# Performance work log

Hardware: AMD Instinct MI355X
Metric: run time of the kernel (lower is better)

The kernel has to match this reference:

```python
import jax, jax.numpy as jnp
import numpy as np

DIM = 1024
NUM_HEADS = 16
HEAD_DIM = DIM // NUM_HEADS
SCALE = HEAD_DIM ** (-0.5)


def alibi_slopes(num_heads):
    x = (2 ** 8) ** (1.0 / num_heads)
    return jnp.array([1.0 / x ** (i + 1) for i in range(num_heads)], dtype=jnp.float32)


def setup_inputs() -> dict:
    key = jax.random.key(0)
    ks = jax.random.split(key, 6)
    B, N = 2, 2048
    x = jax.random.normal(ks[0], (B, N, DIM), dtype=jnp.float32)
    s = DIM ** -0.5
    Wq = jax.random.normal(ks[1], (DIM, DIM), dtype=jnp.float32) * s
    Wk = jax.random.normal(ks[2], (DIM, DIM), dtype=jnp.float32) * s
    Wv = jax.random.normal(ks[3], (DIM, DIM), dtype=jnp.float32) * s
    Wp = jax.random.normal(ks[4], (DIM, DIM), dtype=jnp.float32) * s
    bp = jnp.zeros((DIM,), dtype=jnp.float32)
    return {"x": x, "Wq": Wq, "Wk": Wk, "Wv": Wv, "Wp": Wp, "bp": bp}


def reference(x, Wq, Wk, Wv, Wp, bp):
    B, N, C = x.shape
    H, D = NUM_HEADS, HEAD_DIM
    # Linear layers use torch convention: y = x @ W.T
    q = (x @ Wq.T).reshape(B, N, H, D).transpose(0, 2, 1, 3)  # [B,H,N,D]
    k = (x @ Wk.T).reshape(B, N, H, D).transpose(0, 2, 1, 3)
    v = (x @ Wv.T).reshape(B, N, H, D).transpose(0, 2, 1, 3)
    # ALiBi bias: slopes[h] * (j - i), shape [H,N,N]
    rel = (jnp.arange(N)[None, :] - jnp.arange(N)[:, None]).astype(jnp.float32)
    bias = alibi_slopes(H)[:, None, None] * rel  # [H,N,N]
    # NOTE: original code DIVIDES by scale (= head_dim**-0.5), i.e. multiplies by sqrt(D)
    score = jnp.einsum("bhnd,bhmd->bhnm", q, k) / SCALE + bias[None]
    attn = jax.nn.softmax(score, axis=-1)
    out = jnp.einsum("bhnm,bhmd->bhnd", attn, v)
    out = out.transpose(0, 2, 1, 3).reshape(B, N, C)
    return out @ Wp.T + bp
```

## Files before the change

kernel.cpp:

```cpp
#include <hip/hip_runtime.h>
#include <hip/hip_bf16.h>
#include <cstdint>
#include <cstddef>

#define BB 2
#define NN 2048
#define CC 1024
#define HH 16
#define DD 64
#define MM (BB*NN)

typedef __attribute__((ext_vector_type(8))) _Float16 half8;
typedef __attribute__((ext_vector_type(4))) _Float16 half4;
typedef __attribute__((ext_vector_type(4))) float f32x4;

__device__ __forceinline__ float exp2_fast(float x) {
    float r; asm("v_exp_f32 %0, %1" : "=v"(r) : "v"(x)); return r;
}

__device__ __forceinline__ void gl_lds16(const void* g, void* l) {
    __builtin_amdgcn_global_load_lds(
        (const __attribute__((address_space(1))) unsigned int*)g,
        (__attribute__((address_space(3))) unsigned int*)l, 16, 0, 0);
}

__global__ __launch_bounds__(256) void cvtAll(
    const float* __restrict__ x, const float* __restrict__ wq,
    const float* __restrict__ wk, const float* __restrict__ wv,
    const float* __restrict__ wp, _Float16* __restrict__ X16,
    _Float16* __restrict__ W16) {
    const int NX4 = MM * CC / 4;
    const int NW4 = CC * CC / 4;
    int i = blockIdx.x * 256 + threadIdx.x;
    const float4* src;
    half4* dst;
    if (i < NX4) {
        src = (const float4*)x + i;
        dst = (half4*)X16 + i;
    } else {
        int j = i - NX4;
        int s = j >> 18, off = j & (NW4 - 1);
        const float* wsel = (s == 0) ? wq : (s == 1) ? wk : (s == 2) ? wv : wp;
        src = (const float4*)wsel + off;
        dst = (half4*)(W16 + (size_t)s * CC * CC) + off;
    }
    float4 v = *src;
    half4 h = { (_Float16)v.x, (_Float16)v.y, (_Float16)v.z, (_Float16)v.w };
    *dst = h;
}

__global__ __launch_bounds__(256) void gemmQKV(
    const _Float16* __restrict__ A, const _Float16* __restrict__ B,
    _Float16* __restrict__ QH, _Float16* __restrict__ KH,
    _Float16* __restrict__ VT, float qscale) {
    __shared__ _Float16 sA[128 * 64];
    __shared__ _Float16 sB[128 * 64];
    const int K = CC;

    const int t = threadIdx.x;
    const int id = blockIdx.y * gridDim.x + blockIdx.x;
    const int xcd = id & 7, kk = id >> 3;
    const int bm = xcd * 4 + (kk & 3);
    const int bn = kk >> 2;
    const int w = t >> 6, lane = t & 63;
    const int wr = (w >> 1) * 64, wc = (w & 1) * 64;
    const int lr = lane & 15, lg = lane >> 4;

    f32x4 acc[4][4];
#pragma unroll
    for (int a = 0; a < 4; ++a)
#pragma unroll
        for (int b2 = 0; b2 < 4; ++b2)
#pragma unroll
            for (int e = 0; e < 4; ++e) acc[a][b2][e] = 0.f;

    for (int kt = 0; kt < K; kt += 64) {
#pragma unroll
        for (int p = 0; p < 4; ++p) {
            int u = p * 256 + t;
            int rowu = u >> 3, su = (u & 7) ^ (rowu & 7);
            gl_lds16(A + (size_t)(bm * 128 + rowu) * K + kt + su * 8, sA + u * 8);
            gl_lds16(B + (size_t)(bn * 128 + rowu) * K + kt + su * 8, sB + u * 8);
        }
        __syncthreads();

#pragma unroll
        for (int c = 0; c < 2; ++c) {
            half8 af[4], bf[4];
#pragma unroll
            for (int f = 0; f < 4; ++f) {
                int ra = wr + f * 16 + lr;
                af[f] = *(const half8*)((const char*)sA + ((ra * 128 + c * 64 + lg * 16) ^ ((ra & 7) << 4)));
                int rb = wc + f * 16 + lr;
                bf[f] = *(const half8*)((const char*)sB + ((rb * 128 + c * 64 + lg * 16) ^ ((rb & 7) << 4)));
            }
#pragma unroll
            for (int fi = 0; fi < 4; ++fi)
#pragma unroll
                for (int fj = 0; fj < 4; ++fj)
                    acc[fi][fj] = __builtin_amdgcn_mfma_f32_16x16x32_f16(af[fi], bf[fj], acc[fi][fj], 0, 0, 0);
        }
        __syncthreads();
    }

#pragma unroll
    for (int fi = 0; fi < 4; ++fi)
#pragma unroll
        for (int fj = 0; fj < 4; ++fj) {
            int col = bn * 128 + wc + fj * 16 + lr;
            int sel = col >> 10, c10 = col & 1023;
            int h2 = c10 >> 6, d2 = c10 & 63;
            int rowb = bm * 128 + wr + fi * 16 + lg * 4;
            int b2 = rowb >> 11, n2 = rowb & (NN - 1);
            if (sel == 0) {
#pragma unroll
                for (int e = 0; e < 4; ++e)
                    QH[((size_t)(b2 * HH + h2) * NN + n2 + e) * DD + d2] =
                        (_Float16)(acc[fi][fj][e] * qscale);
            } else if (sel == 1) {
#pragma unroll
                for (int e = 0; e < 4; ++e)
                    KH[((size_t)(b2 * HH + h2) * NN + n2 + e) * DD + d2] =
                        (_Float16)acc[fi][fj][e];
            } else {
                half4 pk = { (_Float16)acc[fi][fj][0], (_Float16)acc[fi][fj][1],
                             (_Float16)acc[fi][fj][2], (_Float16)acc[fi][fj][3] };
                *(half4*)(VT + ((size_t)(b2 * HH + h2) * DD + d2) * NN + n2) = pk;
            }
        }
}

__global__ __launch_bounds__(256) void gemmPROJ(
    const _Float16* __restrict__ A, const _Float16* __restrict__ B,
    const float* __restrict__ bias, float* __restrict__ Cout) {
    __shared__ _Float16 sA[128 * 64];
    __shared__ _Float16 sB[64 * 64];
    const int K = CC, N = CC;

    const int t = threadIdx.x;
    const int id = blockIdx.y * gridDim.x + blockIdx.x;
    const int xcd = id & 7, kk = id >> 3;
    const int bm = xcd * 4 + (kk & 3);
    const int bn = kk >> 2;
    const int w = t >> 6, lane = t & 63;
    const int wr = (w >> 1) * 64, wc = (w & 1) * 32;
    const int lr = lane & 15, lg = lane >> 4;

    f32x4 acc[4][2];
#pragma unroll
    for (int a = 0; a < 4; ++a)
#pragma unroll
        for (int b2 = 0; b2 < 2; ++b2)
#pragma unroll
            for (int e = 0; e < 4; ++e) acc[a][b2][e] = 0.f;

    for (int kt = 0; kt < K; kt += 64) {
#pragma unroll
        for (int p = 0; p < 4; ++p) {
            int u = p * 256 + t;
            int rowu = u >> 3, su = (u & 7) ^ (rowu & 7);
            gl_lds16(A + (size_t)(bm * 128 + rowu) * K + kt + su * 8, sA + u * 8);
        }
#pragma unroll
        for (int p = 0; p < 2; ++p) {
            int u = p * 256 + t;
            int rowu = u >> 3, su = (u & 7) ^ (rowu & 7);
            gl_lds16(B + (size_t)(bn * 64 + rowu) * K + kt + su * 8, sB + u * 8);
        }
        __syncthreads();

#pragma unroll
        for (int c = 0; c < 2; ++c) {
            half8 af[4], bf[2];
#pragma unroll
            for (int f = 0; f < 4; ++f) {
                int ra = wr + f * 16 + lr;
                af[f] = *(const half8*)((const char*)sA + ((ra * 128 + c * 64 + lg * 16) ^ ((ra & 7) << 4)));
            }
#pragma unroll
            for (int f = 0; f < 2; ++f) {
                int rb = wc + f * 16 + lr;
                bf[f] = *(const half8*)((const char*)sB + ((rb * 128 + c * 64 + lg * 16) ^ ((rb & 7) << 4)));
            }
#pragma unroll
            for (int fi = 0; fi < 4; ++fi)
#pragma unroll
                for (int fj = 0; fj < 2; ++fj)
                    acc[fi][fj] = __builtin_amdgcn_mfma_f32_16x16x32_f16(af[fi], bf[fj], acc[fi][fj], 0, 0, 0);
        }
        __syncthreads();
    }

#pragma unroll
    for (int fi = 0; fi < 4; ++fi)
#pragma unroll
        for (int fj = 0; fj < 2; ++fj)
#pragma unroll
            for (int e = 0; e < 4; ++e) {
                int row = bm * 128 + wr + fi * 16 + lg * 4 + e;
                int col = bn * 64 + wc + fj * 16 + lr;
                Cout[(size_t)row * N + col] = acc[fi][fj][e] + bias[col];
            }
}

__global__ __launch_bounds__(512, 4) void attnPC(
    const _Float16* __restrict__ Qh, const _Float16* __restrict__ Kh,
    const _Float16* __restrict__ Vt, _Float16* __restrict__ AO) {
    __shared__ _Float16 sK[2][64 * 64];
    __shared__ _Float16 sV[2][64 * 64];
    __shared__ _Float16 sP[2][4][32 * 64];
    __shared__ float sAl[2][4][32];
    __shared__ float sL[4][32];

    const int t = threadIdx.x, w = t >> 6, lane = t & 63;
    const int lr = lane & 15, lg = lane >> 4;
    const int bh = blockIdx.x, qb = blockIdx.y;
    const int b = bh >> 4, h = bh & 15;
    const int i0 = qb * 128;
    const size_t baseND = (size_t)bh * NN * DD;
    const size_t baseDN = (size_t)bh * DD * NN;
    const bool isProd = (w < 4);
    const int pw = w & 3;

    const float slope2 = exp2f(-0.5f * (float)(h + 1)) * 1.44269504f;
    const float s64v = slope2 * 64.f;
    const float s16v = slope2 * 16.f;
    float cini0[4];
#pragma unroll
    for (int e = 0; e < 4; ++e) cini0[e] = slope2 * (float)(lg * 4 + e);

    auto stageK = [&](int buf, int jt) {
        int rowu = t >> 3, su = (t & 7) ^ (rowu & 7);
        gl_lds16(Kh + baseND + (size_t)(jt * 64 + rowu) * DD + su * 8, &sK[buf][t * 8]);
    };
    auto stageV = [&](int buf, int jt) {
        int rowu = t >> 3, su = (t & 7) ^ (rowu & 7);
        gl_lds16(Vt + baseDN + (size_t)rowu * NN + jt * 64 + su * 8, &sV[buf][t * 8]);
    };

    half8 qf[2][2];
    float m_run[2], l_run[2], tbp = 0.f;
    f32x4 accO[2][4];

    if (isProd) {
#pragma unroll
        for (int u = 0; u < 2; ++u) {
            const size_t qoff = baseND + (size_t)(i0 + pw * 32 + u * 16 + lr) * DD;
            qf[u][0] = *(const half8*)(Qh + qoff + 0 * 32 + lg * 8);
            qf[u][1] = *(const half8*)(Qh + qoff + 1 * 32 + lg * 8);
        }
        m_run[0] = m_run[1] = -INFINITY;
        l_run[0] = l_run[1] = 0.f;
    } else {
#pragma unroll
        for (int u = 0; u < 2; ++u)
#pragma unroll
            for (int c2 = 0; c2 < 4; ++c2)
                accO[u][c2][0] = accO[u][c2][1] = accO[u][c2][2] = accO[u][c2][3] = 0.f;
    }

    auto prodStep = [&](int pb, int kb) {
        f32x4 s0[4], s1[4];
#pragma unroll
        for (int ct = 0; ct < 4; ++ct) {
            float base = tbp + s16v * (float)ct;
#pragma unroll
            for (int e = 0; e < 4; ++e) { s0[ct][e] = base + cini0[e]; s1[ct][e] = s0[ct][e]; }
        }
        __builtin_amdgcn_s_setprio(1);
#pragma unroll
        for (int ct = 0; ct < 4; ++ct)
#pragma unroll
            for (int c = 0; c < 2; ++c) {
                int row = ct * 16 + lr;
                half8 kf = *(const half8*)((const char*)&sK[kb][0] +
                    ((row * 128 + c * 64 + lg * 16) ^ ((row & 7) << 4)));
                s0[ct] = __builtin_amdgcn_mfma_f32_16x16x32_f16(kf, qf[0][c], s0[ct], 0, 0, 0);
                s1[ct] = __builtin_amdgcn_mfma_f32_16x16x32_f16(kf, qf[1][c], s1[ct], 0, 0, 0);
            }
        __builtin_amdgcn_s_setprio(0);
#pragma unroll
        for (int u = 0; u < 2; ++u) {
            f32x4* s = u ? s1 : s0;
            float x0 = fmaxf(fmaxf(s[0][0], s[0][1]), fmaxf(s[0][2], s[0][3]));
            float x1 = fmaxf(fmaxf(s[1][0], s[1][1]), fmaxf(s[1][2], s[1][3]));
            float x2 = fmaxf(fmaxf(s[2][0], s[2][1]), fmaxf(s[2][2], s[2][3]));
            float x3 = fmaxf(fmaxf(s[3][0], s[3][1]), fmaxf(s[3][2], s[3][3]));
            float mx = fmaxf(fmaxf(x0, x1), fmaxf(x2, x3));
            mx = fmaxf(mx, __shfl_xor(mx, 16, 64));
            mx = fmaxf(mx, __shfl_xor(mx, 32, 64));
            float mnew = fmaxf(m_run[u], mx);
            float al = exp2_fast(m_run[u] - mnew);
#pragma unroll
            for (int ct = 0; ct < 4; ++ct)
#pragma unroll
                for (int e = 0; e < 4; ++e) s[ct][e] = exp2_fast(s[ct][e] - mnew);
            float y0 = (s[0][0] + s[0][1]) + (s[0][2] + s[0][3]);
            float y1 = (s[1][0] + s[1][1]) + (s[1][2] + s[1][3]);
            float y2 = (s[2][0] + s[2][1]) + (s[2][2] + s[2][3]);
            float y3 = (s[3][0] + s[3][1]) + (s[3][2] + s[3][3]);
            float sum = (y0 + y1) + (y2 + y3);
            sum += __shfl_xor(sum, 16, 64);
            sum += __shfl_xor(sum, 32, 64);
            m_run[u] = mnew;
            l_run[u] = l_run[u] * al + sum;
            int row = u * 16 + lr;
#pragma unroll
            for (int ct = 0; ct < 4; ++ct) {
                unsigned plo = __builtin_bit_cast(unsigned,
                    __builtin_amdgcn_cvt_pkrtz(s[ct][0], s[ct][1]));
                unsigned phi = __builtin_bit_cast(unsigned,
                    __builtin_amdgcn_cvt_pkrtz(s[ct][2], s[ct][3]));
                uint2 pk = { plo, phi };
                *(uint2*)((char*)sP[pb][pw] + ((row * 128 + ct * 32 + lg * 8) ^ ((lr & 7) << 4))) = pk;
            }
            if (lg == 0) sAl[pb][pw][row] = al;
        }
        tbp += s64v;
    };

    auto consStep = [&](int vb) {
        float al0 = sAl[vb][pw][lr];
        float al1 = sAl[vb][pw][16 + lr];
#pragma unroll
        for (int c2 = 0; c2 < 4; ++c2)
#pragma unroll
            for (int e = 0; e < 4; ++e) { accO[0][c2][e] *= al0; accO[1][c2][e] *= al1; }
        half8 pb0[2], pb1[2];
#pragma unroll
        for (int c = 0; c < 2; ++c) {
            pb0[c] = *(const half8*)((const char*)sP[vb][pw] +
                ((lr * 128 + c * 64 + lg * 16) ^ ((lr & 7) << 4)));
            pb1[c] = *(const half8*)((const char*)sP[vb][pw] +
                (((16 + lr) * 128 + c * 64 + lg * 16) ^ ((lr & 7) << 4)));
        }
        __builtin_amdgcn_s_setprio(1);
#pragma unroll
        for (int ctd = 0; ctd < 4; ++ctd)
#pragma unroll
            for (int c = 0; c < 2; ++c) {
                int row = ctd * 16 + lr;
                half8 vf = *(const half8*)((const char*)&sV[vb][0] +
                    ((row * 128 + c * 64 + lg * 16) ^ ((row & 7) << 4)));
                accO[0][ctd] = __builtin_amdgcn_mfma_f32_16x16x32_f16(vf, pb0[c], accO[0][ctd], 0, 0, 0);
                accO[1][ctd] = __builtin_amdgcn_mfma_f32_16x16x32_f16(vf, pb1[c], accO[1][ctd], 0, 0, 0);
            }
        __builtin_amdgcn_s_setprio(0);
    };

    stageK(0, 0); stageK(1, 1); stageV(0, 0);
    __syncthreads();
    if (isProd) prodStep(0, 0);
    __syncthreads();

    for (int j = 0; j < 32; ++j) {
        if (j + 2 < 32) stageK(j & 1, j + 2);
        if (j + 1 < 32) stageV((j + 1) & 1, j + 1);
        if (isProd) {
            if (j + 1 < 32) prodStep((j + 1) & 1, (j + 1) & 1);
        } else {
            consStep(j & 1);
        }
        __syncthreads();
    }

    if (isProd && lg == 0) { sL[pw][lr] = l_run[0]; sL[pw][16 + lr] = l_run[1]; }
    __syncthreads();
    if (!isProd) {
#pragma unroll
        for (int u = 0; u < 2; ++u) {
            float rl = 1.0f / sL[pw][u * 16 + lr];
            const size_t obase = ((size_t)b * NN + i0 + pw * 32 + u * 16 + lr) * CC + h * DD;
#pragma unroll
            for (int ctd = 0; ctd < 4; ++ctd) {
                half4 ov = { (_Float16)(accO[u][ctd][0] * rl), (_Float16)(accO[u][ctd][1] * rl),
                             (_Float16)(accO[u][ctd][2] * rl), (_Float16)(accO[u][ctd][3] * rl) };
                *(half4*)(AO + obase + ctd * 16 + lg * 4) = ov;
            }
        }
    }
}

extern "C" void kernel_launch(void* const* d_in, const int* in_sizes, int n_in,
                              void* d_out, int out_size, void* d_ws, size_t ws_size,
                              hipStream_t stream) {
    const float* x  = (const float*)d_in[0];
    const float* Wq = (const float*)d_in[1];
    const float* Wk = (const float*)d_in[2];
    const float* Wv = (const float*)d_in[3];
    const float* Wp = (const float*)d_in[4];
    const float* bp = (const float*)d_in[5];
    float* out = (float*)d_out;

    char* ws = (char*)d_ws;
    const size_t MB = 1024 * 1024;
    _Float16* X16 = (_Float16*)(ws + 0 * MB);
    _Float16* W16 = (_Float16*)(ws + 8 * MB);
    _Float16* QH  = (_Float16*)(ws + 16 * MB);
    _Float16* KH  = (_Float16*)(ws + 24 * MB);
    _Float16* VT  = (_Float16*)(ws + 32 * MB);
    _Float16* AO  = (_Float16*)(ws + 40 * MB);
    _Float16* WP16 = W16 + 3 * 1024 * 1024;

    cvtAll<<<8192, 256, 0, stream>>>(x, Wq, Wk, Wv, Wp, X16, W16);

    const float QSCALE = 8.0f * 1.44269504f;
    gemmQKV<<<dim3(3 * CC / 128, MM / 128), 256, 0, stream>>>(X16, W16, QH, KH, VT, QSCALE);

    attnPC<<<dim3(BB * HH, NN / 128), 512, 0, stream>>>(QH, KH, VT, AO);

    gemmPROJ<<<dim3(CC / 64, MM / 128), 256, 0, stream>>>(AO, WP16, bp, out);
}
```

Measured before the change: 137.8 us.

## Move softmax row-sum to consumer MFMA and hoist ALiBi bias init out of loop

The softmax denominator is now computed on the consumer warps with extra MFMAs against a ones vector over the fp16 P tile, instead of the producer doing a sum reduction with shuffles. The constant per-column ALiBi bias becomes a precomputed accumulator init, and the per-tile offset is folded into the max/shift scalar. This lightens the producer's VALU and shuffle work on the critical path and drops the final LDS exchange and barrier. The cost is a few extra MFMAs per consumer step, and the row sum now comes from rounded fp16 probabilities.

```diff
diff --git a/kernel.cpp b/kernel.cpp
--- a/kernel.cpp
+++ b/kernel.cpp
@@ -210,7 +210,6 @@
     __shared__ _Float16 sV[2][64 * 64];
     __shared__ _Float16 sP[2][4][32 * 64];
     __shared__ float sAl[2][4][32];
-    __shared__ float sL[4][32];
 
     const int t = threadIdx.x, w = t >> 6, lane = t & 63;
     const int lr = lane & 15, lg = lane >> 4;
@@ -224,10 +223,6 @@
 
     const float slope2 = exp2f(-0.5f * (float)(h + 1)) * 1.44269504f;
     const float s64v = slope2 * 64.f;
-    const float s16v = slope2 * 16.f;
-    float cini0[4];
-#pragma unroll
-    for (int e = 0; e < 4; ++e) cini0[e] = slope2 * (float)(lg * 4 + e);
 
     auto stageK = [&](int buf, int jt) {
         int rowu = t >> 3, su = (t & 7) ^ (rowu & 7);
@@ -239,8 +234,10 @@
     };
 
     half8 qf[2][2];
-    float m_run[2], l_run[2], tbp = 0.f;
+    f32x4 cfull[4];
+    float m_run[2], tbp = 0.f;
     f32x4 accO[2][4];
+    f32x4 accL[2];
 
     if (isProd) {
 #pragma unroll
@@ -249,35 +246,37 @@
             qf[u][0] = *(const half8*)(Qh + qoff + 0 * 32 + lg * 8);
             qf[u][1] = *(const half8*)(Qh + qoff + 1 * 32 + lg * 8);
         }
+#pragma unroll
+        for (int ct = 0; ct < 4; ++ct)
+#pragma unroll
+            for (int e = 0; e < 4; ++e)
+                cfull[ct][e] = slope2 * (float)(ct * 16 + lg * 4 + e);
         m_run[0] = m_run[1] = -INFINITY;
-        l_run[0] = l_run[1] = 0.f;
     } else {
 #pragma unroll
-        for (int u = 0; u < 2; ++u)
+        for (int u = 0; u < 2; ++u) {
+            accL[u][0] = accL[u][1] = accL[u][2] = accL[u][3] = 0.f;
 #pragma unroll
             for (int c2 = 0; c2 < 4; ++c2)
                 accO[u][c2][0] = accO[u][c2][1] = accO[u][c2][2] = accO[u][c2][3] = 0.f;
+        }
     }
 
     auto prodStep = [&](int pb, int kb) {
         f32x4 s0[4], s1[4];
+        __builtin_amdgcn_s_setprio(1);
 #pragma unroll
         for (int ct = 0; ct < 4; ++ct) {
-            float base = tbp + s16v * (float)ct;
-#pragma unroll
-            for (int e = 0; e < 4; ++e) { s0[ct][e] = base + cini0[e]; s1[ct][e] = s0[ct][e]; }
-        }
-        __builtin_amdgcn_s_setprio(1);
-#pragma unroll
-        for (int ct = 0; ct < 4; ++ct)
-#pragma unroll
-            for (int c = 0; c < 2; ++c) {
-                int row = ct * 16 + lr;
-                half8 kf = *(const half8*)((const char*)&sK[kb][0] +
-                    ((row * 128 + c * 64 + lg * 16) ^ ((row & 7) << 4)));
-                s0[ct] = __builtin_amdgcn_mfma_f32_16x16x32_f16(kf, qf[0][c], s0[ct], 0, 0, 0);
-                s1[ct] = __builtin_amdgcn_mfma_f32_16x16x32_f16(kf, qf[1][c], s1[ct], 0, 0, 0);
-            }
+            int row = ct * 16 + lr;
+            half8 kf0 = *(const half8*)((const char*)&sK[kb][0] +
+                ((row * 128 + 0 * 64 + lg * 16) ^ ((row & 7) << 4)));
+            s0[ct] = __builtin_amdgcn_mfma_f32_16x16x32_f16(kf0, qf[0][0], cfull[ct], 0, 0, 0);
+            s1[ct] = __builtin_amdgcn_mfma_f32_16x16x32_f16(kf0, qf[1][0], cfull[ct], 0, 0, 0);
+            half8 kf1 = *(const half8*)((const char*)&sK[kb][0] +
+                ((row * 128 + 1 * 64 + lg * 16) ^ ((row & 7) << 4)));
+            s0[ct] = __builtin_amdgcn_mfma_f32_16x16x32_f16(kf1, qf[0][1], s0[ct], 0, 0, 0);
+            s1[ct] = __builtin_amdgcn_mfma_f32_16x16x32_f16(kf1, qf[1][1], s1[ct], 0, 0, 0);
+        }
         __builtin_amdgcn_s_setprio(0);
 #pragma unroll
         for (int u = 0; u < 2; ++u) {
@@ -289,28 +288,20 @@
             float mx = fmaxf(fmaxf(x0, x1), fmaxf(x2, x3));
             mx = fmaxf(mx, __shfl_xor(mx, 16, 64));
             mx = fmaxf(mx, __shfl_xor(mx, 32, 64));
-            float mnew = fmaxf(m_run[u], mx);
+            float mxt = mx + tbp;
+            float mnew = fmaxf(m_run[u], mxt);
             float al = exp2_fast(m_run[u] - mnew);
-#pragma unroll
-            for (int ct = 0; ct < 4; ++ct)
-#pragma unroll
-                for (int e = 0; e < 4; ++e) s[ct][e] = exp2_fast(s[ct][e] - mnew);
-            float y0 = (s[0][0] + s[0][1]) + (s[0][2] + s[0][3]);
-            float y1 = (s[1][0] + s[1][1]) + (s[1][2] + s[1][3]);
-            float y2 = (s[2][0] + s[2][1]) + (s[2][2] + s[2][3]);
-            float y3 = (s[3][0] + s[3][1]) + (s[3][2] + s[3][3]);
-            float sum = (y0 + y1) + (y2 + y3);
-            sum += __shfl_xor(sum, 16, 64);
-            sum += __shfl_xor(sum, 32, 64);
+            float msh = mnew - tbp;
             m_run[u] = mnew;
-            l_run[u] = l_run[u] * al + sum;
             int row = u * 16 + lr;
 #pragma unroll
             for (int ct = 0; ct < 4; ++ct) {
-                unsigned plo = __builtin_bit_cast(unsigned,
-                    __builtin_amdgcn_cvt_pkrtz(s[ct][0], s[ct][1]));
-                unsigned phi = __builtin_bit_cast(unsigned,
-                    __builtin_amdgcn_cvt_pkrtz(s[ct][2], s[ct][3]));
+                float p0 = exp2_fast(s[ct][0] - msh);
+                float p1 = exp2_fast(s[ct][1] - msh);
+                float p2 = exp2_fast(s[ct][2] - msh);
+                float p3 = exp2_fast(s[ct][3] - msh);
+                unsigned plo = __builtin_bit_cast(unsigned, __builtin_amdgcn_cvt_pkrtz(p0, p1));
+                unsigned phi = __builtin_bit_cast(unsigned, __builtin_amdgcn_cvt_pkrtz(p2, p3));
                 uint2 pk = { plo, phi };
                 *(uint2*)((char*)sP[pb][pw] + ((row * 128 + ct * 32 + lg * 8) ^ ((lr & 7) << 4))) = pk;
             }
@@ -326,6 +317,8 @@
         for (int c2 = 0; c2 < 4; ++c2)
 #pragma unroll
             for (int e = 0; e < 4; ++e) { accO[0][c2][e] *= al0; accO[1][c2][e] *= al1; }
+#pragma unroll
+        for (int e = 0; e < 4; ++e) { accL[0][e] *= al0; accL[1][e] *= al1; }
         half8 pb0[2], pb1[2];
 #pragma unroll
         for (int c = 0; c < 2; ++c) {
@@ -334,6 +327,8 @@
             pb1[c] = *(const half8*)((const char*)sP[vb][pw] +
                 (((16 + lr) * 128 + c * 64 + lg * 16) ^ ((lr & 7) << 4)));
         }
+        const half8 ones = { (_Float16)1.f, (_Float16)1.f, (_Float16)1.f, (_Float16)1.f,
+                             (_Float16)1.f, (_Float16)1.f, (_Float16)1.f, (_Float16)1.f };
         __builtin_amdgcn_s_setprio(1);
 #pragma unroll
         for (int ctd = 0; ctd < 4; ++ctd)
@@ -345,6 +340,11 @@
                 accO[0][ctd] = __builtin_amdgcn_mfma_f32_16x16x32_f16(vf, pb0[c], accO[0][ctd], 0, 0, 0);
                 accO[1][ctd] = __builtin_amdgcn_mfma_f32_16x16x32_f16(vf, pb1[c], accO[1][ctd], 0, 0, 0);
             }
+#pragma unroll
+        for (int c = 0; c < 2; ++c) {
+            accL[0] = __builtin_amdgcn_mfma_f32_16x16x32_f16(ones, pb0[c], accL[0], 0, 0, 0);
+            accL[1] = __builtin_amdgcn_mfma_f32_16x16x32_f16(ones, pb1[c], accL[1], 0, 0, 0);
+        }
         __builtin_amdgcn_s_setprio(0);
     };
 
@@ -364,12 +364,10 @@
         __syncthreads();
     }
 
-    if (isProd && lg == 0) { sL[pw][lr] = l_run[0]; sL[pw][16 + lr] = l_run[1]; }
-    __syncthreads();
     if (!isProd) {
 #pragma unroll
         for (int u = 0; u < 2; ++u) {
-            float rl = 1.0f / sL[pw][u * 16 + lr];
+            float rl = 1.0f / accL[u][0];
             const size_t obase = ((size_t)b * NN + i0 + pw * 32 + u * 16 + lr) * CC + h * DD;
 #pragma unroll
             for (int ctd = 0; ctd < 4; ++ctd) {
```

New measurement: 160.5 us. 16.5% more time.
